# Kernel tuning notes

Hardware: AMD Instinct MI355X
Metric: run time of the kernel (lower is better)

The kernel has to match this reference:

```python
import jax, jax.numpy as jnp
import numpy as np

# MoE config (matches init_kwargs)
T = 16384   # tokens
H = 1024    # hidden size
I = 1024    # intermediate size per expert
E = 8       # n_experts
TOPK = 2
RENORMALIZE = True


def setup_inputs() -> dict:
    key = jax.random.key(0)
    ks = jax.random.split(key, 6)
    x = jax.random.normal(ks[0], (T, H), dtype=jnp.float32)
    gating_output = jax.random.normal(ks[1], (T, E), dtype=jnp.float32)
    # fp8-quantized weights simulated as their integer-grid values in fp32;
    # dequant = q * per-expert scalar scale (normalize_e4m3fn_to_native_float8 path)
    w1 = jax.random.normal(ks[2], (E, 2 * I, H), dtype=jnp.float32)  # fused [gate; up]
    w2 = jax.random.normal(ks[3], (E, H, I), dtype=jnp.float32)      # down_proj
    w1_scale = jax.random.uniform(ks[4], (E,), dtype=jnp.float32, minval=0.01, maxval=0.05)
    w2_scale = jax.random.uniform(ks[5], (E,), dtype=jnp.float32, minval=0.01, maxval=0.05)
    return {"x": x, "gating_output": gating_output, "w1": w1, "w2": w2,
            "w1_scale": w1_scale, "w2_scale": w2_scale}


def _moe(x, gating_output, w1, w2, w1_scale, w2_scale):
    # softmax scoring -> top-k routing (use_grouped_topk=False)
    probs = jax.nn.softmax(gating_output, axis=-1)              # [T, E]
    topk_w, topk_idx = jax.lax.top_k(probs, TOPK)               # [T, K]
    if RENORMALIZE:
        topk_w = topk_w / jnp.sum(topk_w, axis=-1, keepdims=True)
    out = jnp.zeros_like(x)
    for e in range(E):  # fixed small expert count: grouped-GEMM reference
        w1e = w1[e] * w1_scale[e]                               # dequant [2I, H]
        w2e = w2[e] * w2_scale[e]                               # dequant [H, I]
        gate = x @ w1e[:I].T                                    # [T, I]
        up = x @ w1e[I:].T                                      # [T, I]
        h = jax.nn.silu(gate) * up                              # SwiGLU
        y = h @ w2e.T                                           # [T, H]
        # per-token routing weight for this expert (0 if not routed)
        coef = jnp.sum(jnp.where(topk_idx == e, topk_w, 0.0), axis=-1)  # [T]
        out = out + coef[:, None] * y
    return out


def reference(x, gating_output, w1, w2, w1_scale, w2_scale):
    return _moe(x, gating_output, w1, w2, w1_scale, w2_scale)
```

## Files before the change

kernel.cpp:

```cpp
#include <hip/hip_runtime.h>
#include <hip/hip_bf16.h>

#define T_TOK 16384
#define H_DIM 1024
#define I_DIM 1024
#define E_NUM 8
#define NPAIR (T_TOK * 2)
#define BM 256
#define BK 64
#define KITER 16
#define MAX_MT (NPAIR / BM + E_NUM)

typedef float v4f __attribute__((ext_vector_type(4)));
typedef float v16f __attribute__((ext_vector_type(16)));
typedef short v8s __attribute__((ext_vector_type(8)));

__device__ __forceinline__ unsigned short f2bf(float f) {
    unsigned int u = __float_as_uint(f);
    unsigned int r = (u + 0x7fffu + ((u >> 16) & 1u)) >> 16;
    return (unsigned short)r;
}
__device__ __forceinline__ float bf2f(unsigned short s) {
    return __uint_as_float(((unsigned int)s) << 16);
}

__device__ __forceinline__ void gl_lds16(const void* g, void* l) {
    __builtin_amdgcn_global_load_lds(
        (const __attribute__((address_space(1))) void*)g,
        (__attribute__((address_space(3))) void*)l, 16, 0, 0);
}

__device__ __forceinline__ int swz(int row, int unit) {
    return row * 64 + ((unit ^ (row & 7)) << 3);
}

__device__ __forceinline__ int blkA_of(int w, int j) {
    int idx = 2 * w + (j & 1);
    int blk = idx + ((idx >= 8) ? 8 : 0);
    return blk + ((j >= 2) ? 8 : 0);
}
__device__ __forceinline__ int blkB_of(int w, int j) {
    int idx = 2 * w + (j & 1);
    int blk = (idx >> 2) * 8 + (idx & 3);
    return blk + ((j >= 2) ? 4 : 0);
}

__device__ __forceinline__ void rd_a(const unsigned short* lAc, int rbase, int lane, v8s a[2][4]) {
#pragma unroll
    for (int i = 0; i < 2; i++)
#pragma unroll
        for (int ks = 0; ks < 4; ks++)
            a[i][ks] = *(const v8s*)(lAc + swz(rbase + i * 32 + (lane & 31), 2 * ks + (lane >> 5)));
}
__device__ __forceinline__ void rd_b(const unsigned short* lBc, int rbase, int lane, v8s b[4]) {
#pragma unroll
    for (int ks = 0; ks < 4; ks++)
        b[ks] = *(const v8s*)(lBc + swz(rbase + (lane & 31), 2 * ks + (lane >> 5)));
}
__device__ __forceinline__ void mfma8(const v8s a[2][4], const v8s b[4], v16f* c0, v16f* c1) {
#pragma unroll
    for (int ks = 0; ks < 4; ks++) {
        *c0 = __builtin_amdgcn_mfma_f32_32x32x16_bf16(a[0][ks], b[ks], *c0, 0, 0, 0);
        *c1 = __builtin_amdgcn_mfma_f32_32x32x16_bf16(a[1][ks], b[ks], *c1, 0, 0, 0);
    }
}

__global__ void k_route(const float* __restrict__ gating,
                        int* __restrict__ tokExp, float* __restrict__ tokW,
                        int* __restrict__ counts) {
    int t = blockIdx.x * 256 + threadIdx.x;
    int lane = threadIdx.x & 63;
    float g[E_NUM];
#pragma unroll
    for (int e = 0; e < E_NUM; e++) g[e] = gating[t * E_NUM + e];
    int i0 = 0; float v0 = g[0];
#pragma unroll
    for (int e = 1; e < E_NUM; e++) if (g[e] > v0) { v0 = g[e]; i0 = e; }
    int i1 = -1; float v1 = -1e30f;
#pragma unroll
    for (int e = 0; e < E_NUM; e++) if (e != i0 && g[e] > v1) { v1 = g[e]; i1 = e; }
    float w0 = 1.f / (1.f + __expf(v1 - v0));
    tokExp[2 * t] = i0; tokExp[2 * t + 1] = i1;
    tokW[2 * t] = w0;   tokW[2 * t + 1] = 1.f - w0;
#pragma unroll
    for (int e = 0; e < E_NUM; e++) {
        unsigned long long mA = __ballot(i0 == e);
        unsigned long long mB = __ballot(i1 == e);
        int c = __popcll(mA) + __popcll(mB);
        if (lane == 0 && c) atomicAdd(&counts[e], c);
    }
}

__global__ void k_scan(const int* __restrict__ counts, int* __restrict__ offsets,
                       int* __restrict__ tileOff, int* __restrict__ cursor) {
    if (threadIdx.x == 0 && blockIdx.x == 0) {
        int o = 0, to = 0;
        for (int e = 0; e < E_NUM; e++) {
            offsets[e] = o; tileOff[e] = to; cursor[e] = o;
            o += counts[e];
            to += (counts[e] + BM - 1) / BM;
        }
        offsets[E_NUM] = o; tileOff[E_NUM] = to;
    }
}

__global__ void k_scatter(const int* __restrict__ tokExp, const float* __restrict__ tokW,
                          int* __restrict__ cursor,
                          int* __restrict__ pairTok, float* __restrict__ pairW,
                          int* __restrict__ invMap) {
    int t = blockIdx.x * 256 + threadIdx.x;
    int lane = threadIdx.x & 63;
#pragma unroll
    for (int k = 0; k < 2; k++) {
        int e = tokExp[2 * t + k];
        int pos = 0;
#pragma unroll
        for (int ex = 0; ex < E_NUM; ex++) {
            unsigned long long m = __ballot(e == ex);
            if (m) {
                int leader = __builtin_ctzll(m);
                int base = 0;
                if (lane == leader) base = atomicAdd(&cursor[ex], __popcll(m));
                base = __shfl(base, leader);
                if (e == ex) pos = base + __popcll(m & ((1ull << lane) - 1ull));
            }
        }
        pairTok[pos] = t;
        pairW[pos] = tokW[2 * t + k];
        invMap[2 * t + k] = pos;
    }
}

__global__ void k_cvt_x(const float* __restrict__ src, unsigned short* __restrict__ dst) {
    size_t i4 = ((size_t)blockIdx.x * 256 + threadIdx.x) * 4;
    float4 v = *(const float4*)(src + i4);
    ushort4 o;
    o.x = f2bf(v.x); o.y = f2bf(v.y); o.z = f2bf(v.z); o.w = f2bf(v.w);
    *(ushort4*)(dst + i4) = o;
}

__global__ void k_cvt_w(const float* __restrict__ src, unsigned short* __restrict__ dst,
                        const float* __restrict__ scale, int shift) {
    size_t i4 = ((size_t)blockIdx.x * 256 + threadIdx.x) * 4;
    float s = scale[i4 >> shift];
    float4 v = *(const float4*)(src + i4);
    ushort4 o;
    o.x = f2bf(v.x * s); o.y = f2bf(v.y * s); o.z = f2bf(v.z * s); o.w = f2bf(v.w * s);
    *(ushort4*)(dst + i4) = o;
}

#define STG_A(buf, j, k0) gl_lds16(aSrc[j] + (k0) + lcs, &lA[buf][aoff[j]])
#define STG_B(buf, j, k0) gl_lds16(bSrc[j] + (k0) + lcs, &lB[buf][boff[j]])

#define GEMM_MAINLOOP                                                          \
    for (int T = 0; T < KITER; T++) {                                          \
        int cur = T & 1;                                                       \
        const unsigned short* lAc = lA[cur];                                   \
        const unsigned short* lBc = lB[cur];                                   \
        int k2 = (T + 2) * BK;                                                 \
        bool s2 = (T + 2 < KITER);                                             \
                                            \
        rd_a(lAc, wm * 128, lane, a);                                          \
        rd_b(lBc, bbase, lane, b0);                                            \
        __builtin_amdgcn_s_barrier();                                          \
        __builtin_amdgcn_s_setprio(1);                                         \
        mfma8(a, b0, &acc[0][0], &acc[1][0]);                                  \
        __builtin_amdgcn_s_setprio(0);                                         \
        __builtin_amdgcn_s_barrier();                                          \
                                     \
        rd_b(lBc, bbase + 32, lane, b1);                                       \
        if (s2) { STG_B(cur, 0, k2); STG_B(cur, 1, k2); }                      \
        __builtin_amdgcn_s_barrier();                                          \
        __builtin_amdgcn_s_setprio(1);                                         \
        mfma8(a, b1, &acc[0][1], &acc[1][1]);                                  \
        __builtin_amdgcn_s_setprio(0);                                         \
        __builtin_amdgcn_s_barrier();                                          \
                                   \
        rd_a(lAc, wm * 128 + 64, lane, a);                                     \
        if (s2) { STG_B(cur, 2, k2); STG_B(cur, 3, k2); }                      \
        __builtin_amdgcn_s_barrier();                                          \
        __builtin_amdgcn_s_setprio(1);                                         \
        mfma8(a, b0, &acc[2][0], &acc[3][0]);                                  \
        __builtin_amdgcn_s_setprio(0);                                         \
        __builtin_amdgcn_s_barrier();                                          \
                          \
        if (s2) {                                                              \
            STG_A(cur, 0, k2); STG_A(cur, 1, k2);                              \
            STG_A(cur, 2, k2); STG_A(cur, 3, k2);                              \
            asm volatile("s_waitcnt vmcnt(8)" ::: "memory");                    \
        } else if (T + 1 < KITER) {                                            \
            asm volatile("s_waitcnt vmcnt(0)" ::: "memory");                    \
        }                                                                      \
        __builtin_amdgcn_sched_barrier(0);                                     \
        __builtin_amdgcn_s_barrier();                                          \
        __builtin_amdgcn_s_setprio(1);                                         \
        mfma8(a, b1, &acc[2][1], &acc[3][1]);                                  \
        __builtin_amdgcn_s_setprio(0);                                         \
        __builtin_amdgcn_s_barrier();                                          \
        __builtin_amdgcn_sched_barrier(0);                                     \
    }

__global__ __launch_bounds__(512, 2)
void k_gemm1(const unsigned short* __restrict__ xbf,
             const unsigned short* __restrict__ w1bf,
             const int* __restrict__ pairTok,
             const int* __restrict__ offsets, const int* __restrict__ tileOff,
             unsigned short* __restrict__ hbuf) {
    __shared__ unsigned short lA[2][BM * BK];
    __shared__ unsigned short lB[2][BM * BK];

    int mt = blockIdx.x;
    if (mt >= tileOff[E_NUM]) return;
    int e = 0;
    while (mt >= tileOff[e + 1]) e++;
    int row0 = offsets[e] + (mt - tileOff[e]) * BM;
    int valid = offsets[e + 1] - row0; if (valid > BM) valid = BM;

    int nt = blockIdx.y;
    int tid = threadIdx.x;
    int lane = tid & 63, wave = tid >> 6;
    int wm = wave >> 2, wn = wave & 3;
    int lr = lane >> 3;
    int lcs = ((lane & 7) ^ lr) * 8;
    int bbase = (wn & 1) * 64 + (wn >> 1) * 128;

    const unsigned short* wg = w1bf + (size_t)e * 2 * I_DIM * H_DIM + (size_t)(nt * 128) * H_DIM;
    const unsigned short* wu = wg + (size_t)I_DIM * H_DIM;

    const unsigned short* aSrc[4];
    const unsigned short* bSrc[4];
    int aoff[4], boff[4];
#pragma unroll
    for (int j = 0; j < 4; j++) {
        int ab = blkA_of(wave, j), bb = blkB_of(wave, j);
        aoff[j] = ab * 512; boff[j] = bb * 512;
        int ra = ab * 8 + lr;
        int rc = ra < valid ? ra : valid - 1;
        aSrc[j] = xbf + (size_t)pairTok[row0 + rc] * H_DIM;
        int rb = bb * 8 + lr;
        bSrc[j] = (rb < 128) ? (wg + (size_t)rb * H_DIM) : (wu + (size_t)(rb - 128) * H_DIM);
    }

    v16f acc[4][2];
#pragma unroll
    for (int i = 0; i < 4; i++) { acc[i][0] = (v16f)0.f; acc[i][1] = (v16f)0.f; }

#pragma unroll
    for (int j = 0; j < 4; j++) STG_A(0, j, 0);
#pragma unroll
    for (int j = 0; j < 4; j++) STG_B(0, j, 0);
#pragma unroll
    for (int j = 0; j < 4; j++) STG_B(1, j, BK);
#pragma unroll
    for (int j = 0; j < 4; j++) STG_A(1, j, BK);
    asm volatile("s_waitcnt vmcnt(8)" ::: "memory");
    __builtin_amdgcn_sched_barrier(0);
    __builtin_amdgcn_s_barrier();

    v8s a[2][4], b0[4], b1[4];
#pragma unroll 2
    GEMM_MAINLOOP

    __syncthreads();
    unsigned short* uLds = &lA[0][0];
    int half = lane >> 5, c = lane & 31;
    if (wn >= 2) {
#pragma unroll
        for (int i = 0; i < 4; i++)
#pragma unroll
            for (int r = 0; r < 16; r++) {
                int row = wm * 128 + i * 32 + (r & 3) + 8 * (r >> 2) + 4 * half;
#pragma unroll
                for (int j = 0; j < 2; j++)
                    uLds[row * 128 + (wn - 2) * 64 + j * 32 + c] = f2bf(acc[i][j][r]);
            }
    }
    __syncthreads();
    if (wn < 2) {
#pragma unroll
        for (int i = 0; i < 4; i++)
#pragma unroll
            for (int r = 0; r < 16; r++) {
                int row = wm * 128 + i * 32 + (r & 3) + 8 * (r >> 2) + 4 * half;
                if (row < valid) {
                    size_t base = (size_t)(row0 + row) * I_DIM + nt * 128;
#pragma unroll
                    for (int j = 0; j < 2; j++) {
                        float g = acc[i][j][r];
                        float uu = bf2f(uLds[row * 128 + wn * 64 + j * 32 + c]);
                        float s = g / (1.f + __expf(-g));
                        hbuf[base + wn * 64 + j * 32 + c] = f2bf(s * uu);
                    }
                }
            }
    }
}

__global__ __launch_bounds__(512, 2)
void k_gemm2(const unsigned short* __restrict__ hbuf,
             const unsigned short* __restrict__ w2bf,
             const float* __restrict__ pairW,
             const int* __restrict__ offsets, const int* __restrict__ tileOff,
             unsigned short* __restrict__ ybuf) {
    __shared__ unsigned short lA[2][BM * BK];
    __shared__ unsigned short lB[2][BM * BK];

    int mt = blockIdx.x;
    if (mt >= tileOff[E_NUM]) return;
    int e = 0;
    while (mt >= tileOff[e + 1]) e++;
    int row0 = offsets[e] + (mt - tileOff[e]) * BM;
    int valid = offsets[e + 1] - row0; if (valid > BM) valid = BM;

    int nt = blockIdx.y;
    int tid = threadIdx.x;
    int lane = tid & 63, wave = tid >> 6;
    int wm = wave >> 2, wn = wave & 3;
    int lr = lane >> 3;
    int lcs = ((lane & 7) ^ lr) * 8;
    int bbase = wn * 64;

    const unsigned short* w2e = w2bf + (size_t)e * H_DIM * I_DIM + (size_t)(nt * 256) * I_DIM;

    const unsigned short* aSrc[4];
    const unsigned short* bSrc[4];
    int aoff[4], boff[4];
#pragma unroll
    for (int j = 0; j < 4; j++) {
        int ab = blkA_of(wave, j), bb = blkB_of(wave, j);
        aoff[j] = ab * 512; boff[j] = bb * 512;
        int ra = ab * 8 + lr;
        int rc = ra < valid ? ra : valid - 1;
        aSrc[j] = hbuf + (size_t)(row0 + rc) * I_DIM;
        bSrc[j] = w2e + (size_t)(bb * 8 + lr) * I_DIM;
    }

    v16f acc[4][2];
#pragma unroll
    for (int i = 0; i < 4; i++) { acc[i][0] = (v16f)0.f; acc[i][1] = (v16f)0.f; }

#pragma unroll
    for (int j = 0; j < 4; j++) STG_A(0, j, 0);
#pragma unroll
    for (int j = 0; j < 4; j++) STG_B(0, j, 0);
#pragma unroll
    for (int j = 0; j < 4; j++) STG_B(1, j, BK);
#pragma unroll
    for (int j = 0; j < 4; j++) STG_A(1, j, BK);
    asm volatile("s_waitcnt vmcnt(8)" ::: "memory");
    __builtin_amdgcn_sched_barrier(0);
    __builtin_amdgcn_s_barrier();

    v8s a[2][4], b0[4], b1[4];
#pragma unroll 2
    GEMM_MAINLOOP

    int half = lane >> 5, c = lane & 31;
#pragma unroll
    for (int i = 0; i < 4; i++)
#pragma unroll
        for (int r = 0; r < 16; r++) {
            int row = wm * 128 + i * 32 + (r & 3) + 8 * (r >> 2) + 4 * half;
            if (row < valid) {
                int pos = row0 + row;
                float coef = pairW[pos];
                unsigned short* orow = ybuf + (size_t)pos * H_DIM + nt * 256;
#pragma unroll
                for (int j = 0; j < 2; j++)
                    orow[bbase + j * 32 + c] = f2bf(coef * acc[i][j][r]);
            }
        }
}

__global__ __launch_bounds__(256)
void k_reduce(const unsigned short* __restrict__ ybuf,
              const int* __restrict__ invMap,
              float* __restrict__ out) {
    int t = blockIdx.x;
    int p0 = invMap[2 * t], p1 = invMap[2 * t + 1];
    int c4 = threadIdx.x * 4;
    ushort4 a = *(const ushort4*)(ybuf + (size_t)p0 * H_DIM + c4);
    ushort4 b = *(const ushort4*)(ybuf + (size_t)p1 * H_DIM + c4);
    float4 o;
    o.x = bf2f(a.x) + bf2f(b.x);
    o.y = bf2f(a.y) + bf2f(b.y);
    o.z = bf2f(a.z) + bf2f(b.z);
    o.w = bf2f(a.w) + bf2f(b.w);
    *(float4*)(out + (size_t)t * H_DIM + c4) = o;
}

extern "C" void kernel_launch(void* const* d_in, const int* in_sizes, int n_in,
                              void* d_out, int out_size, void* d_ws, size_t ws_size,
                              hipStream_t stream) {
    const float* x      = (const float*)d_in[0];
    const float* gating = (const float*)d_in[1];
    const float* w1     = (const float*)d_in[2];
    const float* w2     = (const float*)d_in[3];
    const float* w1s    = (const float*)d_in[4];
    const float* w2s    = (const float*)d_in[5];
    float* out = (float*)d_out;

    char* ws = (char*)d_ws;
    size_t off = 0;
    auto alloc = [&](size_t bytes) { void* p = ws + off; off += (bytes + 255) & ~(size_t)255; return p; };
    unsigned short* xbf  = (unsigned short*)alloc((size_t)T_TOK * H_DIM * 2);
    unsigned short* w1bf = (unsigned short*)alloc((size_t)E_NUM * 2 * I_DIM * H_DIM * 2);
    unsigned short* w2bf = (unsigned short*)alloc((size_t)E_NUM * H_DIM * I_DIM * 2);
    unsigned short* hbuf = (unsigned short*)alloc((size_t)NPAIR * I_DIM * 2);
    unsigned short* ybuf = (unsigned short*)alloc((size_t)NPAIR * H_DIM * 2);
    int*   pairTok  = (int*)alloc(NPAIR * 4);
    float* pairW    = (float*)alloc(NPAIR * 4);
    int*   tokExp   = (int*)alloc(NPAIR * 4);
    float* tokW     = (float*)alloc(NPAIR * 4);
    int*   invMap   = (int*)alloc(NPAIR * 4);
    int*   counts   = (int*)alloc(64);
    int*   offsets  = (int*)alloc(64);
    int*   tileOff  = (int*)alloc(64);
    int*   cursor   = (int*)alloc(64);

    hipMemsetAsync(counts, 0, 64, stream);

    k_route<<<T_TOK / 256, 256, 0, stream>>>(gating, tokExp, tokW, counts);
    k_scan<<<1, 64, 0, stream>>>(counts, offsets, tileOff, cursor);
    k_scatter<<<T_TOK / 256, 256, 0, stream>>>(tokExp, tokW, cursor, pairTok, pairW, invMap);
    k_cvt_x<<<(T_TOK * H_DIM / 4) / 256, 256, 0, stream>>>(x, xbf);
    k_cvt_w<<<(E_NUM * 2 * I_DIM * H_DIM / 4) / 256, 256, 0, stream>>>(w1, w1bf, w1s, 21);
    k_cvt_w<<<(E_NUM * H_DIM * I_DIM / 4) / 256, 256, 0, stream>>>(w2, w2bf, w2s, 20);

    dim3 g1(MAX_MT, I_DIM / 128);
    k_gemm1<<<g1, 512, 0, stream>>>(xbf, w1bf, pairTok, offsets, tileOff, hbuf);
    dim3 g2(MAX_MT, H_DIM / 256);
    k_gemm2<<<g2, 512, 0, stream>>>(hbuf, w2bf, pairW, offsets, tileOff, ybuf);
    k_reduce<<<T_TOK, 256, 0, stream>>>(ybuf, invMap, out);
}
```

Measured before the change: 644.7 us.

## Restage GEMM prefetch pipeline with split A loads and peeled tail iterations

```diff
diff --git a/kernel.cpp b/kernel.cpp
--- a/kernel.cpp
+++ b/kernel.cpp
@@ -149,56 +149,68 @@
     *(ushort4*)(dst + i4) = o;
 }
 
-#define STG_A(buf, j, k0) gl_lds16(aSrc[j] + (k0) + lcs, &lA[buf][aoff[j]])
-#define STG_B(buf, j, k0) gl_lds16(bSrc[j] + (k0) + lcs, &lB[buf][boff[j]])
-
-#define GEMM_MAINLOOP                                                          \
-    for (int T = 0; T < KITER; T++) {                                          \
-        int cur = T & 1;                                                       \
-        const unsigned short* lAc = lA[cur];                                   \
-        const unsigned short* lBc = lB[cur];                                   \
-        int k2 = (T + 2) * BK;                                                 \
-        bool s2 = (T + 2 < KITER);                                             \
-                                            \
-        rd_a(lAc, wm * 128, lane, a);                                          \
-        rd_b(lBc, bbase, lane, b0);                                            \
-        __builtin_amdgcn_s_barrier();                                          \
-        __builtin_amdgcn_s_setprio(1);                                         \
-        mfma8(a, b0, &acc[0][0], &acc[1][0]);                                  \
-        __builtin_amdgcn_s_setprio(0);                                         \
-        __builtin_amdgcn_s_barrier();                                          \
-                                     \
-        rd_b(lBc, bbase + 32, lane, b1);                                       \
-        if (s2) { STG_B(cur, 0, k2); STG_B(cur, 1, k2); }                      \
-        __builtin_amdgcn_s_barrier();                                          \
-        __builtin_amdgcn_s_setprio(1);                                         \
-        mfma8(a, b1, &acc[0][1], &acc[1][1]);                                  \
-        __builtin_amdgcn_s_setprio(0);                                         \
-        __builtin_amdgcn_s_barrier();                                          \
-                                   \
-        rd_a(lAc, wm * 128 + 64, lane, a);                                     \
-        if (s2) { STG_B(cur, 2, k2); STG_B(cur, 3, k2); }                      \
-        __builtin_amdgcn_s_barrier();                                          \
-        __builtin_amdgcn_s_setprio(1);                                         \
-        mfma8(a, b0, &acc[2][0], &acc[3][0]);                                  \
-        __builtin_amdgcn_s_setprio(0);                                         \
-        __builtin_amdgcn_s_barrier();                                          \
-                          \
-        if (s2) {                                                              \
-            STG_A(cur, 0, k2); STG_A(cur, 1, k2);                              \
-            STG_A(cur, 2, k2); STG_A(cur, 3, k2);                              \
-            asm volatile("s_waitcnt vmcnt(8)" ::: "memory");                    \
-        } else if (T + 1 < KITER) {                                            \
-            asm volatile("s_waitcnt vmcnt(0)" ::: "memory");                    \
-        }                                                                      \
-        __builtin_amdgcn_sched_barrier(0);                                     \
-        __builtin_amdgcn_s_barrier();                                          \
-        __builtin_amdgcn_s_setprio(1);                                         \
-        mfma8(a, b1, &acc[2][1], &acc[3][1]);                                  \
-        __builtin_amdgcn_s_setprio(0);                                         \
-        __builtin_amdgcn_s_barrier();                                          \
-        __builtin_amdgcn_sched_barrier(0);                                     \
-    }
+#define STG_A2(buf, jlo, k0)                                                  \
+    do { gl_lds16(aSrc[jlo] + (k0) + lcs, &lA[buf][aoff[jlo]]);               \
+         gl_lds16(aSrc[(jlo)+1] + (k0) + lcs, &lA[buf][aoff[(jlo)+1]]); } while (0)
+#define STG_B2(buf, jlo, k0)                                                  \
+    do { gl_lds16(bSrc[jlo] + (k0) + lcs, &lB[buf][boff[jlo]]);               \
+         gl_lds16(bSrc[(jlo)+1] + (k0) + lcs, &lB[buf][boff[(jlo)+1]]); } while (0)
+
+#define PHASE_SYNC_MFMA(BVEC, C0, C1)                                         \
+    __builtin_amdgcn_s_barrier();                                             \
+    asm volatile("s_waitcnt lgkmcnt(0)" ::: "memory");                        \
+    __builtin_amdgcn_sched_barrier(0);                                        \
+    __builtin_amdgcn_s_setprio(1);                                            \
+    mfma8(a, BVEC, C0, C1);                                                   \
+    __builtin_amdgcn_s_setprio(0);                                            \
+    __builtin_amdgcn_s_barrier();
+
+#define TILE_BODY(cur, Tv, DOA1, DOT2)                                        \
+    do {                                                                      \
+        const unsigned short* lAc = lA[cur];                                  \
+        const unsigned short* lBc = lB[cur];                                  \
+                                                            \
+        rd_a(lAc, wm * 128, lane, a);                                         \
+        rd_b(lBc, bbase, lane, b0);                                           \
+        if (DOA1) STG_A2((cur) ^ 1, 2, ((Tv) + 1) * BK);                      \
+        asm volatile("s_waitcnt lgkmcnt(8)" ::: "memory");                    \
+        PHASE_SYNC_MFMA(b0, &acc[0][0], &acc[1][0])                           \
+                                                            \
+        rd_b(lBc, bbase + 32, lane, b1);                                      \
+        if (DOT2) STG_B2(cur, 0, ((Tv) + 2) * BK);                            \
+        PHASE_SYNC_MFMA(b1, &acc[0][1], &acc[1][1])                           \
+                                                            \
+        rd_a(lAc, wm * 128 + 64, lane, a);                                    \
+        if (DOT2) STG_B2(cur, 2, ((Tv) + 2) * BK);                            \
+        PHASE_SYNC_MFMA(b0, &acc[2][0], &acc[3][0])                           \
+                                                            \
+        if (DOT2) {                                                           \
+            STG_A2(cur, 0, ((Tv) + 2) * BK);                                  \
+            asm volatile("s_waitcnt vmcnt(6)" ::: "memory");                  \
+        } else {                                                              \
+            asm volatile("s_waitcnt vmcnt(0)" ::: "memory");                  \
+        }                                                                     \
+        __builtin_amdgcn_sched_barrier(0);                                    \
+        __builtin_amdgcn_s_barrier();                                         \
+        __builtin_amdgcn_s_setprio(1);                                        \
+        mfma8(a, b1, &acc[2][1], &acc[3][1]);                                 \
+        __builtin_amdgcn_s_setprio(0);                                        \
+        __builtin_amdgcn_s_barrier();                                         \
+    } while (0)
+
+#define GEMM_PROLOGUE                                                         \
+    STG_A2(0, 0, 0); STG_A2(0, 2, 0); STG_B2(0, 0, 0); STG_B2(0, 2, 0);       \
+    STG_B2(1, 0, BK); STG_B2(1, 2, BK); STG_A2(1, 0, BK);                     \
+    asm volatile("s_waitcnt vmcnt(6)" ::: "memory");                          \
+    __builtin_amdgcn_sched_barrier(0);                                        \
+    __builtin_amdgcn_s_barrier();
+
+#define GEMM_MAINLOOP                                                         \
+    GEMM_PROLOGUE                                                             \
+    _Pragma("unroll 2")                                                       \
+    for (int T = 0; T < KITER - 2; T++) TILE_BODY(T & 1, T, 1, 1);            \
+    TILE_BODY(0, KITER - 2, 1, 0);         \
+    TILE_BODY(1, KITER - 1, 0, 0);
 
 __global__ __launch_bounds__(512, 2)
 void k_gemm1(const unsigned short* __restrict__ xbf,
@@ -245,20 +257,7 @@
 #pragma unroll
     for (int i = 0; i < 4; i++) { acc[i][0] = (v16f)0.f; acc[i][1] = (v16f)0.f; }
 
-#pragma unroll
-    for (int j = 0; j < 4; j++) STG_A(0, j, 0);
-#pragma unroll
-    for (int j = 0; j < 4; j++) STG_B(0, j, 0);
-#pragma unroll
-    for (int j = 0; j < 4; j++) STG_B(1, j, BK);
-#pragma unroll
-    for (int j = 0; j < 4; j++) STG_A(1, j, BK);
-    asm volatile("s_waitcnt vmcnt(8)" ::: "memory");
-    __builtin_amdgcn_sched_barrier(0);
-    __builtin_amdgcn_s_barrier();
-
     v8s a[2][4], b0[4], b1[4];
-#pragma unroll 2
     GEMM_MAINLOOP
 
     __syncthreads();
@@ -339,20 +338,7 @@
 #pragma unroll
     for (int i = 0; i < 4; i++) { acc[i][0] = (v16f)0.f; acc[i][1] = (v16f)0.f; }
 
-#pragma unroll
-    for (int j = 0; j < 4; j++) STG_A(0, j, 0);
-#pragma unroll
-    for (int j = 0; j < 4; j++) STG_B(0, j, 0);
-#pragma unroll
-    for (int j = 0; j < 4; j++) STG_B(1, j, BK);
-#pragma unroll
-    for (int j = 0; j < 4; j++) STG_A(1, j, BK);
-    asm volatile("s_waitcnt vmcnt(8)" ::: "memory");
-    __builtin_amdgcn_sched_barrier(0);
-    __builtin_amdgcn_s_barrier();
-
     v8s a[2][4], b0[4], b1[4];
-#pragma unroll 2
     GEMM_MAINLOOP
 
     int half = lane >> 5, c = lane & 31;
```

Measured after the change: 659.8 us. 2.3% more time.
